# Kernel tuning notes

Hardware: AMD Instinct MI355X
Metric: run time of the kernel (lower is better)

Reference implementation:

```python
import jax, jax.numpy as jnp
import numpy as np

SIGMA = 1.0
DELTA = 1.0
TOPK = 10
TOPK_HALF = 5  # int(np.around(TOPK / 2))
N, D = 4096, 512
N_IDS = 2048  # N / view


def _l2_normalize(x, eps=1e-12):
    n = jnp.linalg.norm(x, axis=1, keepdims=True)
    return x / jnp.maximum(n, eps)


def _cdist(a, b):
    # Euclidean distance with a sqrt that is safe at 0 (diagonal).
    sq = (jnp.sum(a * a, 1)[:, None] + jnp.sum(b * b, 1)[None, :]
          - 2.0 * (a @ b.T))
    sq = jnp.maximum(sq, 0.0)
    return jnp.where(sq > 0, jnp.sqrt(jnp.where(sq > 0, sq, 1.0)), 0.0)


def setup_inputs() -> dict:
    key = jax.random.key(0)
    k1, k2, k3 = jax.random.split(key, 3)
    s_emb = jax.random.normal(k1, (N, D), dtype=jnp.float32)
    t_emb = jax.random.normal(k2, (N, D), dtype=jnp.float32)
    idx = jax.random.randint(k3, (N,), 0, N_IDS, dtype=jnp.int64)
    return {"s_emb": s_emb, "t_emb": t_emb, "idx": idx}


def reference(s_emb, t_emb, idx):
    n = s_emb.shape[0]
    s = _l2_normalize(s_emb)          # disable_mu=True
    t = _l2_normalize(t_emb)

    S_dist = _cdist(s, s)
    S_dist = S_dist / jnp.mean(S_dist, axis=1, keepdims=True)

    # --- teacher-side neighbor graph (no_grad in original) ---
    T_dist = _cdist(t, t)
    W_P = jnp.exp(-(T_dist ** 2) / SIGMA)                      # [N,N]
    same = idx[:, None] == idx[None, :]
    W_P_copy = jnp.where(same, 1.0, W_P)
    _, topk_index = jax.lax.top_k(W_P_copy, TOPK)              # [N,k]
    topk_half_index = topk_index[:, :TOPK_HALF]                # [N,k/2]

    rows = jnp.arange(n)[:, None]
    W_NN = jnp.zeros((n, n), jnp.float32).at[rows, topk_index].set(1.0)
    V = ((W_NN + W_NN.T) / 2.0 == 1.0).astype(jnp.float32)     # mutual kNN

    # Vectorized form of the per-row nonzero gather-reduce loop:
    # W_C_tilda[i,j] = V[i,j] * (sum_l V[i,l] V[j,l]) / |{l: V[i,l]>0}|
    row_cnt = jnp.sum(V, axis=1)                               # [N]
    VV = jnp.einsum('il,jl->ij', V, V)                         # [N,N]
    W_C_tilda = jnp.where(V > 0, VV / jnp.maximum(row_cnt, 1.0)[:, None], 0.0)

    W_C_hat = jnp.mean(W_C_tilda[topk_half_index], axis=1)     # [N,k/2,N]->[N,N]
    W_C = (W_C_hat + W_C_hat.T) / 2.0
    W = (W_P + W_C) / 2.0

    eye = jnp.eye(n, dtype=jnp.float32)
    pos_weight = W * (1.0 - eye)
    neg_weight = (1.0 - W) * (1.0 - eye)

    pull = jnp.maximum(S_dist, 0.0) ** 2 * pos_weight
    push = jnp.maximum(DELTA - S_dist, 0.0) ** 2 * neg_weight
    loss = (jnp.sum(pull) + jnp.sum(push)) / (n * (n - 1))
    return loss
```

## Files before the change

kernel.cpp:

```cpp
#include <hip/hip_runtime.h>
#include <math.h>

#define N 4096
#define D 512
#define TOPK 10
#define TOPK_HALF 5
#define NT 32
#define TRI_BLOCKS (NT * (NT + 1) / 2)
#define WC_BLOCKS (N * TOPK_HALF / 16)
#define INV_N (1.0f / 4096.0f)
#define TPAD 132

typedef __bf16 bf16;
typedef __bf16 bf16x8 __attribute__((ext_vector_type(8)));
typedef float f32x4 __attribute__((ext_vector_type(4)));
typedef _Float16 f16;
typedef _Float16 f16x4 __attribute__((ext_vector_type(4)));
typedef _Float16 f16x8 __attribute__((ext_vector_type(8)));
typedef unsigned short u16;
typedef unsigned short u16x8 __attribute__((ext_vector_type(8)));
typedef unsigned int u32;

__device__ __forceinline__ void gl_lds16(const void* g, void* l) {
  __builtin_amdgcn_global_load_lds(
      (const __attribute__((address_space(1))) void*)g,
      (__attribute__((address_space(3))) void*)l, 16, 0, 0);
}

__device__ __forceinline__ float f16tof(u16 h) {
  return (float)__builtin_bit_cast(_Float16, h);
}

__global__ __launch_bounds__(256) void k_normalize2(const float* __restrict__ xs,
                                                    const float* __restrict__ xt,
                                                    bf16* __restrict__ ys,
                                                    bf16* __restrict__ yt,
                                                    float* __restrict__ rsq_s,
                                                    float* __restrict__ rsq_t,
                                                    float* __restrict__ rowsum) {
  int b = blockIdx.x;
  int row = b & (N - 1);
  int is_t = b >> 12;
  const float* x = is_t ? xt : xs;
  bf16* y = is_t ? yt : ys;
  float* rowsq = is_t ? rsq_t : rsq_s;
  int tid = threadIdx.x;
  const float* xr = x + (size_t)row * D;
  float v0 = xr[tid], v1 = xr[tid + 256];
  float ss = v0 * v0 + v1 * v1;
  __shared__ float red[4];
  for (int off = 32; off > 0; off >>= 1) ss += __shfl_down(ss, off, 64);
  if ((tid & 63) == 0) red[tid >> 6] = ss;
  __syncthreads();
  float tot = red[0] + red[1] + red[2] + red[3];
  float inv = 1.0f / fmaxf(sqrtf(tot), 1e-12f);
  bf16 b0 = (bf16)(v0 * inv), b1 = (bf16)(v1 * inv);
  bf16* yr = y + (size_t)row * D;
  yr[tid] = b0; yr[tid + 256] = b1;
  float f0 = (float)b0, f1 = (float)b1;
  float s2 = f0 * f0 + f1 * f1;
  for (int off = 32; off > 0; off >>= 1) s2 += __shfl_down(s2, off, 64);
  __syncthreads();
  if ((tid & 63) == 0) red[tid >> 6] = s2;
  __syncthreads();
  if (tid == 0) {
    rowsq[row] = red[0] + red[1] + red[2] + red[3];
    if (!is_t) rowsum[row] = 0.f;
  }
}

__global__ __launch_bounds__(256) void k_dgram3(const bf16* __restrict__ S,
                                                const bf16* __restrict__ T,
                                                const float* __restrict__ rsq_s,
                                                const float* __restrict__ rsq_t,
                                                f16* __restrict__ Gsd,
                                                f16* __restrict__ Gwp,
                                                float* __restrict__ rowsum) {
  __shared__ __align__(16) char sm[128 * TPAD * 2];
  f16* tp = (f16*)sm;

  int z = blockIdx.y;
  const bf16* Y = z ? T : S;
  const float* rsq = z ? rsq_t : rsq_s;
  f16* G = z ? Gwp : Gsd;

  int orig = blockIdx.x;
  int t = (orig & 7) * (TRI_BLOCKS / 8) + (orig >> 3);
  int by = 0;
  while (t >= NT - by) { t -= NT - by; ++by; }
  int bx = by + t;
  bool offdiag = (bx != by);

  int tid = threadIdx.x;
  int lane = tid & 63, w = tid >> 6;
  int wr = w >> 1, wc = w & 1;
  int quad = lane >> 4, c = lane & 15;
  int w1024 = w << 10;

  const char* Jbase = (const char*)(Y + (size_t)(bx * 128) * D);
  const char* Ibase = (const char*)(Y + (size_t)(by * 128) * D);
  int r0 = tid >> 2, q0 = tid & 3;
  int r1 = (tid + 256) >> 2, q1 = (tid + 256) & 3;
  size_t so0 = (size_t)r0 * (D * 2) + q0 * 16;
  size_t so1 = (size_t)r1 * (D * 2) + q1 * 16;

  int jrow = wr * 64 + c;
  int irow = wc * 64 + c;
  int kq = quad * 8;

  char* bA = sm;
  char* bB = sm + 16384;

#define STAGE(buf, kb)                                   \
  {                                                      \
    char* _b = (buf);                                    \
    gl_lds16(Jbase + so0 + (kb), _b + w1024);            \
    gl_lds16(Jbase + so1 + (kb), _b + 4096 + w1024);     \
    gl_lds16(Ibase + so0 + (kb), _b + 8192 + w1024);     \
    gl_lds16(Ibase + so1 + (kb), _b + 12288 + w1024);    \
  }

#define COMPUTE(bufc)                                                          \
  {                                                                            \
    const bf16* Jc = (const bf16*)(bufc);                                      \
    const bf16* Ic = (const bf16*)((bufc) + 8192);                             \
    bf16x8 af[4], bfr[4];                                                      \
    _Pragma("unroll") for (int u = 0; u < 4; ++u)                              \
        af[u] = *(const bf16x8*)&Jc[(jrow + u * 16) * 32 + kq];                \
    _Pragma("unroll") for (int v = 0; v < 4; ++v)                              \
        bfr[v] = *(const bf16x8*)&Ic[(irow + v * 16) * 32 + kq];               \
    _Pragma("unroll") for (int u = 0; u < 4; ++u)                              \
      _Pragma("unroll") for (int v = 0; v < 4; ++v)                            \
        acc[u][v] = __builtin_amdgcn_mfma_f32_16x16x32_bf16(                   \
            af[u], bfr[v], acc[u][v], 0, 0, 0);                                \
  }

  f32x4 acc[4][4] = {};
  STAGE(bA, 0);
  for (int tt = 0; tt < 15; ++tt) {
    char* nb = (tt & 1) ? bA : bB;
    char* cb = (tt & 1) ? bB : bA;
    asm volatile("s_barrier" ::: "memory");
    STAGE(nb, (size_t)(tt + 1) * 64);
    asm volatile("s_waitcnt vmcnt(4)\n\ts_barrier" ::: "memory");
    COMPUTE(cb);
  }
  asm volatile("s_waitcnt vmcnt(0)\n\ts_barrier" ::: "memory");
  COMPUTE(bB);
  __syncthreads();

#undef STAGE
#undef COMPUTE

#pragma unroll
  for (int v = 0; v < 4; ++v) {
    int il = wc * 64 + v * 16 + c;
    int ig = by * 128 + il;
    float ri = rsq[ig];
    float rsv = 0.f;
#pragma unroll
    for (int u = 0; u < 4; ++u) {
      int jl0 = wr * 64 + u * 16 + quad * 4;
      int jb0i = bx * 128 + jl0;
      float4 rj = *(const float4*)(rsq + jb0i);
      const float* rjp = (const float*)&rj;
      f32x4 a = acc[u][v];
      f16x4 st;
      if (z == 0) {
#pragma unroll
        for (int reg = 0; reg < 4; ++reg) {
          float sq = fmaxf(ri + rjp[reg] - 2.0f * a[reg], 0.0f);
          float val = __builtin_amdgcn_sqrtf(sq);
          st[reg] = (_Float16)val;
          rsv += val;
        }
      } else {
#pragma unroll
        for (int reg = 0; reg < 4; ++reg) {
          float sq = fmaxf(ri + rjp[reg] - 2.0f * a[reg], 0.0f);
          st[reg] = (_Float16)__expf(-sq);
        }
      }
      *(f16x4*)(G + (size_t)ig * N + jb0i) = st;
      if (offdiag) {
#pragma unroll
        for (int reg = 0; reg < 4; ++reg) tp[(jl0 + reg) * TPAD + il] = st[reg];
      }
    }
    if (z == 0) {
      rsv += __shfl_xor(rsv, 16, 64);
      rsv += __shfl_xor(rsv, 32, 64);
      if (lane < 16) atomicAdd(&rowsum[ig], rsv);
    }
  }

  if (offdiag) {
    __syncthreads();
    int rloc = tid >> 4;
    int cseg = tid & 15;
#pragma unroll
    for (int it = 0; it < 8; ++it) {
      int jl = it * 16 + rloc;
      int jg = bx * 128 + jl;
      f16x8 v8 = *(f16x8*)&tp[jl * TPAD + cseg * 8];
      *(f16x8*)(G + (size_t)jg * N + by * 128 + cseg * 8) = v8;
      if (z == 0) {
        float csum = 0.f;
#pragma unroll
        for (int e = 0; e < 8; ++e) csum += (float)v8[e];
        csum += __shfl_xor(csum, 1, 64);
        csum += __shfl_xor(csum, 2, 64);
        csum += __shfl_xor(csum, 4, 64);
        csum += __shfl_xor(csum, 8, 64);
        if (cseg == 0) atomicAdd(&rowsum[jg], csum);
      }
    }
  }
}

__global__ __launch_bounds__(256) void k_rowpass(const f16* __restrict__ Gs,
                                                 const f16* __restrict__ Gw,
                                                 const int* __restrict__ ids,
                                                 const float* __restrict__ rowsum,
                                                 int* __restrict__ topk,
                                                 double* __restrict__ pd) {
  __shared__ u32 lds[256 * TOPK];
  __shared__ double dred[4];
  int i = blockIdx.x, tid = threadIdx.x;
  int idi = ids[i];
  float invm = 1.0f / (rowsum[i] * INV_N);
  const u16* srow = (const u16*)(Gs + (size_t)i * N);
  const u16* wrow = (const u16*)(Gw + (size_t)i * N);
  u32 key[16];
  float dsum = 0.f;
  int j0 = tid * 16;
#pragma unroll
  for (int h = 0; h < 2; ++h) {
    int jb = j0 + h * 8;
    u16x8 sv = *(const u16x8*)(srow + jb);
    u16x8 wv = *(const u16x8*)(wrow + jb);
    int4 id0 = *(const int4*)(ids + jb);
    int4 id1 = *(const int4*)(ids + jb + 4);
    const int* idp = (const int*)&id0;
    const int* idp1 = (const int*)&id1;
#pragma unroll
    for (int e = 0; e < 8; ++e) {
      int j = jb + e;
      u16 hw = wv[e];
      float wp = f16tof(hw);
      if (j != i) {
        float sdn = f16tof(sv[e]) * invm;
        float r = fmaxf(1.0f - sdn, 0.0f); r *= r;
        dsum += r + 0.5f * wp * (sdn * sdn - r);
      }
      int idj = (e < 4) ? idp[e] : idp1[e - 4];
      u16 hk = (idj == idi) ? (u16)0x3C00 : hw;
      key[h * 8 + e] = ((u32)hk << 16) | (u32)(4095 - j);
    }
  }
#pragma unroll
  for (int kk = 2; kk <= 16; kk <<= 1) {
#pragma unroll
    for (int jj = kk >> 1; jj > 0; jj >>= 1) {
#pragma unroll
      for (int ii = 0; ii < 16; ++ii) {
        int ll = ii ^ jj;
        if (ll > ii) {
          bool desc = ((ii & kk) == 0);
          u32 a = key[ii], b = key[ll];
          bool sw = desc ? (a < b) : (a > b);
          key[ii] = sw ? b : a;
          key[ll] = sw ? a : b;
        }
      }
    }
  }
  double dl = (double)dsum;
  for (int off = 32; off > 0; off >>= 1) dl += __shfl_down(dl, off, 64);
  if ((tid & 63) == 0) dred[tid >> 6] = dl;
#pragma unroll
  for (int o = 0; o < TOPK; ++o) lds[tid * TOPK + o] = key[o];
  __syncthreads();
  for (int off = 128; off >= 1; off >>= 1) {
    if (tid < off) {
      u32 A[TOPK], B[TOPK];
#pragma unroll
      for (int o = 0; o < TOPK; ++o) {
        A[o] = lds[tid * TOPK + o];
        B[o] = lds[(tid + off) * TOPK + o];
      }
      u32 out[TOPK];
#pragma unroll
      for (int o = 0; o < TOPK; ++o) {
        u32 m = A[o] > B[o] ? A[o] : B[o];
#pragma unroll
        for (int p = 0; p < o; ++p) {
          u32 mn = A[p] < B[o - 1 - p] ? A[p] : B[o - 1 - p];
          m = m > mn ? m : mn;
        }
        out[o] = m;
      }
#pragma unroll
      for (int o = 0; o < TOPK; ++o) lds[tid * TOPK + o] = out[o];
    }
    __syncthreads();
  }
  if (tid == 0) {
#pragma unroll
    for (int o = 0; o < TOPK; ++o)
      topk[i * TOPK + o] = 4095 - (int)(lds[o] & 0xFFFu);
    pd[i] = dred[0] + dred[1] + dred[2] + dred[3];
  }
}

__global__ __launch_bounds__(256) void k_buildV(const int* __restrict__ topk,
                                                int* __restrict__ L,
                                                int* __restrict__ cnt) {
  int tid = threadIdx.x;
  int grp = tid >> 4, gl = tid & 15;
  int i = blockIdx.x * 16 + grp;
  bool act = (gl < TOPK);
  int j = act ? topk[i * TOPK + gl] : 0;
  bool mut = false;
  if (act) {
#pragma unroll
    for (int q = 0; q < TOPK; ++q) mut |= (topk[j * TOPK + q] == i);
  }
  unsigned long long m = __ballot(mut);
  int base = tid & 48;
  unsigned gm = (unsigned)((m >> base) & 0xFFFFull);
  int pos = __popc(gm & ((1u << gl) - 1));
  if (mut) L[i * TOPK + pos] = j;
  if (gl == 0) cnt[i] = __popc(gm);
}

__global__ __launch_bounds__(256) void k_wc(const int* __restrict__ topk,
                                            const int* __restrict__ L,
                                            const int* __restrict__ cnt,
                                            const f16* __restrict__ Gsd,
                                            const float* __restrict__ rowsum,
                                            double* __restrict__ pw) {
  __shared__ double red[16];
  int tid = threadIdx.x;
  int grp = tid >> 4;
  int gl = tid & 15;
  int task = blockIdx.x * 16 + grp;
  int i = task / TOPK_HALF, m = task % TOPK_HALF;
  int r = topk[i * TOPK + m];
  int cr = cnt[r];
  float invmi = 1.0f / (rowsum[i] * INV_N);
  int lval = (gl < cr) ? L[r * TOPK + gl] : -1;
  int Lr[TOPK];
#pragma unroll
  for (int a = 0; a < TOPK; ++a) Lr[a] = __shfl(lval, a, 16);
  float contrib = 0.f;
  if (gl < cr) {
    int j = lval;
    if (j != i) {
      int cj = cnt[j];
      float mj = rowsum[j] * INV_N;
      float sr_ = f16tof(((const u16*)Gsd)[(size_t)i * N + j]);
      int lj[TOPK];
#pragma unroll
      for (int b = 0; b < TOPK; ++b) lj[b] = L[j * TOPK + b];
      int vv = 0;
#pragma unroll
      for (int b = 0; b < TOPK; ++b) {
        if (b < cj) {
#pragma unroll
          for (int a = 0; a < TOPK; ++a)
            vv += ((a < cr) && (lj[b] == Lr[a])) ? 1 : 0;
        }
      }
      float denom = (float)(cr > 1 ? cr : 1);
      float wgt = (float)vv / denom;
      float sdij = sr_ * invmi;
      float sdji = sr_ / mj;
      float Rij = fmaxf(1.0f - sdij, 0.0f); Rij *= Rij;
      float Rji = fmaxf(1.0f - sdji, 0.0f); Rji *= Rji;
      float Fij = sdij * sdij - Rij;
      float Fji = sdji * sdji - Rji;
      contrib = wgt * (Fij + Fji);
    }
  }
  double local = (double)contrib;
  local += __shfl_xor(local, 1, 16);
  local += __shfl_xor(local, 2, 16);
  local += __shfl_xor(local, 4, 16);
  local += __shfl_xor(local, 8, 16);
  if (gl == 0) red[grp] = local;
  __syncthreads();
  if (tid == 0) {
    double s = 0.0;
#pragma unroll
    for (int g = 0; g < 16; ++g) s += red[g];
    pw[blockIdx.x] = s * (1.0 / 20.0);
  }
}

__global__ __launch_bounds__(256) void k_final(const double* __restrict__ pd,
                                               const double* __restrict__ pw,
                                               float* __restrict__ out) {
  int tid = threadIdx.x;
  double s = 0.0;
  for (int i = tid; i < N; i += 256) s += pd[i];
  for (int i = tid; i < WC_BLOCKS; i += 256) s += pw[i];
  for (int off = 32; off > 0; off >>= 1) s += __shfl_down(s, off, 64);
  __shared__ double red[4];
  if ((tid & 63) == 0) red[tid >> 6] = s;
  __syncthreads();
  if (tid == 0)
    out[0] = (float)((red[0] + red[1] + red[2] + red[3]) /
                     ((double)N * (double)(N - 1)));
}

extern "C" void kernel_launch(void* const* d_in, const int* in_sizes, int n_in,
                              void* d_out, int out_size, void* d_ws, size_t ws_size,
                              hipStream_t stream) {
  const float* s_emb = (const float*)d_in[0];
  const float* t_emb = (const float*)d_in[1];
  const int* ids = (const int*)d_in[2];
  float* out = (float*)d_out;

  char* ws = (char*)d_ws;
  size_t off = 0;
  bf16* snorm = (bf16*)(ws + off); off += (size_t)N * D * 2;
  bf16* tnorm = (bf16*)(ws + off); off += (size_t)N * D * 2;
  f16*  Gsd   = (f16*)(ws + off);  off += (size_t)N * N * 2;
  f16*  Gwp   = (f16*)(ws + off);  off += (size_t)N * N * 2;
  float* rsq_s = (float*)(ws + off); off += (size_t)N * 4;
  float* rsq_t = (float*)(ws + off); off += (size_t)N * 4;
  float* rowsum= (float*)(ws + off); off += (size_t)N * 4;
  int*   topk  = (int*)(ws + off);   off += (size_t)N * TOPK * 4;
  int*   L     = (int*)(ws + off);   off += (size_t)N * TOPK * 4;
  int*   cnt   = (int*)(ws + off);   off += (size_t)N * 4;
  off = (off + 15) & ~(size_t)15;
  double* pd   = (double*)(ws + off); off += (size_t)N * 8;
  double* pw   = (double*)(ws + off); off += (size_t)WC_BLOCKS * 8;

  k_normalize2<<<2 * N, 256, 0, stream>>>(s_emb, t_emb, snorm, tnorm,
                                          rsq_s, rsq_t, rowsum);
  k_dgram3<<<dim3(TRI_BLOCKS, 2), 256, 0, stream>>>(snorm, tnorm, rsq_s, rsq_t,
                                                    Gsd, Gwp, rowsum);
  k_rowpass<<<N, 256, 0, stream>>>(Gsd, Gwp, ids, rowsum, topk, pd);
  k_buildV<<<N / 16, 256, 0, stream>>>(topk, L, cnt);
  k_wc<<<WC_BLOCKS, 256, 0, stream>>>(topk, L, cnt, Gsd, rowsum, pw);
  k_final<<<1, 256, 0, stream>>>(pd, pw, out);
}
```

Baseline: 146.9 us.

## Triple-buffer Gram kernel LDS staging and pack two rows per normalize block

The Gram-matrix kernel moves from a double-buffered to a triple-buffered global-to-LDS pipeline. It prefetches two K-steps ahead and waits with vmcnt(8), so load latency is hidden further behind MFMA work. The normalize kernel now has each 128-thread half-block handle one row with float4 loads and bf16x4 stores, which halves the grid and drops a barrier. LDS use per block grows from about 33KB to 48KB, which may lower occupancy.

```diff
diff --git a/kernel.cpp b/kernel.cpp
--- a/kernel.cpp
+++ b/kernel.cpp
@@ -12,6 +12,7 @@
 #define TPAD 132
 
 typedef __bf16 bf16;
+typedef __bf16 bf16x4 __attribute__((ext_vector_type(4)));
 typedef __bf16 bf16x8 __attribute__((ext_vector_type(8)));
 typedef float f32x4 __attribute__((ext_vector_type(4)));
 typedef _Float16 f16;
@@ -39,32 +40,36 @@
                                                     float* __restrict__ rsq_t,
                                                     float* __restrict__ rowsum) {
   int b = blockIdx.x;
-  int row = b & (N - 1);
-  int is_t = b >> 12;
+  int tid = threadIdx.x;
+  int half = tid >> 7;
+  int l = tid & 127;
+  int row2 = 2 * b + half;
+  int is_t = row2 >> 12;
+  int row = row2 & (N - 1);
   const float* x = is_t ? xt : xs;
   bf16* y = is_t ? yt : ys;
   float* rowsq = is_t ? rsq_t : rsq_s;
-  int tid = threadIdx.x;
   const float* xr = x + (size_t)row * D;
-  float v0 = xr[tid], v1 = xr[tid + 256];
-  float ss = v0 * v0 + v1 * v1;
+  float4 v = *(const float4*)(xr + l * 4);
+  float ss = v.x * v.x + v.y * v.y + v.z * v.z + v.w * v.w;
   __shared__ float red[4];
+  __shared__ float red2[4];
   for (int off = 32; off > 0; off >>= 1) ss += __shfl_down(ss, off, 64);
   if ((tid & 63) == 0) red[tid >> 6] = ss;
   __syncthreads();
-  float tot = red[0] + red[1] + red[2] + red[3];
+  float tot = red[half * 2] + red[half * 2 + 1];
   float inv = 1.0f / fmaxf(sqrtf(tot), 1e-12f);
-  bf16 b0 = (bf16)(v0 * inv), b1 = (bf16)(v1 * inv);
-  bf16* yr = y + (size_t)row * D;
-  yr[tid] = b0; yr[tid + 256] = b1;
-  float f0 = (float)b0, f1 = (float)b1;
-  float s2 = f0 * f0 + f1 * f1;
+  bf16x4 bv;
+  bv[0] = (bf16)(v.x * inv); bv[1] = (bf16)(v.y * inv);
+  bv[2] = (bf16)(v.z * inv); bv[3] = (bf16)(v.w * inv);
+  *(bf16x4*)(y + (size_t)row * D + l * 4) = bv;
+  float f0 = (float)bv[0], f1 = (float)bv[1], f2 = (float)bv[2], f3 = (float)bv[3];
+  float s2 = f0 * f0 + f1 * f1 + f2 * f2 + f3 * f3;
   for (int off = 32; off > 0; off >>= 1) s2 += __shfl_down(s2, off, 64);
-  __syncthreads();
-  if ((tid & 63) == 0) red[tid >> 6] = s2;
-  __syncthreads();
-  if (tid == 0) {
-    rowsq[row] = red[0] + red[1] + red[2] + red[3];
+  if ((tid & 63) == 0) red2[tid >> 6] = s2;
+  __syncthreads();
+  if ((tid & 127) == 0) {
+    rowsq[row] = red2[half * 2] + red2[half * 2 + 1];
     if (!is_t) rowsum[row] = 0.f;
   }
 }
@@ -76,7 +81,7 @@
                                                 f16* __restrict__ Gsd,
                                                 f16* __restrict__ Gwp,
                                                 float* __restrict__ rowsum) {
-  __shared__ __align__(16) char sm[128 * TPAD * 2];
+  __shared__ __align__(16) char sm[49152];
   f16* tp = (f16*)sm;
 
   int z = blockIdx.y;
@@ -107,9 +112,6 @@
   int jrow = wr * 64 + c;
   int irow = wc * 64 + c;
   int kq = quad * 8;
-
-  char* bA = sm;
-  char* bB = sm + 16384;
 
 #define STAGE(buf, kb)                                   \
   {                                                      \
@@ -136,17 +138,22 @@
   }
 
   f32x4 acc[4][4] = {};
-  STAGE(bA, 0);
-  for (int tt = 0; tt < 15; ++tt) {
-    char* nb = (tt & 1) ? bA : bB;
-    char* cb = (tt & 1) ? bB : bA;
+  STAGE(sm, 0);
+  STAGE(sm + 16384, 64);
+  int sc = 0, sn = 2;
+  for (int tt = 0; tt < 14; ++tt) {
+    char* nb = sm + (sn << 14);
     asm volatile("s_barrier" ::: "memory");
-    STAGE(nb, (size_t)(tt + 1) * 64);
-    asm volatile("s_waitcnt vmcnt(4)\n\ts_barrier" ::: "memory");
-    COMPUTE(cb);
-  }
+    STAGE(nb, (size_t)(tt + 2) * 64);
+    asm volatile("s_waitcnt vmcnt(8)\n\ts_barrier" ::: "memory");
+    COMPUTE(sm + (sc << 14));
+    sc = (sc == 2) ? 0 : sc + 1;
+    sn = (sn == 2) ? 0 : sn + 1;
+  }
+  asm volatile("s_waitcnt vmcnt(4)\n\ts_barrier" ::: "memory");
+  COMPUTE(sm + 32768);
   asm volatile("s_waitcnt vmcnt(0)\n\ts_barrier" ::: "memory");
-  COMPUTE(bB);
+  COMPUTE(sm);
   __syncthreads();
 
 #undef STAGE
@@ -438,8 +445,8 @@
   double* pd   = (double*)(ws + off); off += (size_t)N * 8;
   double* pw   = (double*)(ws + off); off += (size_t)WC_BLOCKS * 8;
 
-  k_normalize2<<<2 * N, 256, 0, stream>>>(s_emb, t_emb, snorm, tnorm,
-                                          rsq_s, rsq_t, rowsum);
+  k_normalize2<<<N, 256, 0, stream>>>(s_emb, t_emb, snorm, tnorm,
+                                      rsq_s, rsq_t, rowsum);
   k_dgram3<<<dim3(TRI_BLOCKS, 2), 256, 0, stream>>>(snorm, tnorm, rsq_s, rsq_t,
                                                     Gsd, Gwp, rowsum);
   k_rowpass<<<N, 256, 0, stream>>>(Gsd, Gwp, ids, rowsum, topk, pd);
```

After: 145.7 us. Within noise of the previous version (-0.8%).
